# Kernel tuning notes

Hardware: AMD Instinct MI355X
Metric: run time of the kernel (lower is better)

Reference implementation:

```python
import jax, jax.numpy as jnp
import numpy as np

BLOCK = 128      # ModelArgs.block_size
FP8_MAX = 448.0  # e4m3 max, used by act_quant


def setup_inputs() -> dict:
    key = jax.random.key(0)
    k1, k2, k3 = jax.random.split(key, 3)
    M, K, O = 8192, 4096, 4096
    x = jax.random.normal(k1, (M, K), dtype=jnp.float32)
    # 'fp8' weight values (simulated in fp32) and blockwise fp32 scales
    weight = jax.random.normal(k2, (O, K), dtype=jnp.float32)
    w_scale = jax.random.uniform(k3, (O // BLOCK, K // BLOCK), dtype=jnp.float32,
                                 minval=0.5, maxval=1.5)
    return {"x": x, "weight": weight, "w_scale": w_scale}


def reference(x, weight, w_scale):
    M, K = x.shape
    O = weight.shape[0]
    Kb, Ob = K // BLOCK, O // BLOCK

    # --- act_quant: per-(row, k-block) scale = amax/448, quantized vals x/scale ---
    xb = x.reshape(M, Kb, BLOCK)
    sx = jnp.max(jnp.abs(xb), axis=-1, keepdims=True) / FP8_MAX  # [M, Kb, 1]
    xq = xb / sx                                                  # simulated fp8 activations

    # --- weight_dequant: blockwise scale expansion ---
    wdq = (weight.reshape(Ob, BLOCK, Kb, BLOCK) * w_scale[:, None, :, None]).reshape(O, K)

    # --- fp8_gemm: y = (xq * sx) @ wdq^T  (activation scales folded back per block) ---
    xd = (xq * sx).reshape(M, K)
    y = jnp.einsum('mk,ok->mo', xd, wdq)  # [M, O]
    return y
```

## Files before the change

### kernel.cpp

```cpp
#include <hip/hip_runtime.h>

#define M_DIM 8192
#define K_DIM 4096
#define O_DIM 4096
#define QB    128
#define BK    64
#define BMT   256
#define BNT   256

typedef __attribute__((ext_vector_type(8))) short  short8;
typedef __attribute__((ext_vector_type(4))) float  floatx4;

#define AS1 __attribute__((address_space(1)))
#define AS3 __attribute__((address_space(3)))

__device__ __forceinline__ short f2bf(float f) {
    unsigned u = __float_as_uint(f);
    unsigned r = u + 0x7fffu + ((u >> 16) & 1u);
    return (short)(r >> 16);
}

__global__ __launch_bounds__(512) void cvt_fused(const float* __restrict__ x,
                                                 const float* __restrict__ w,
                                                 const float* __restrict__ s,
                                                 short* __restrict__ xb,
                                                 short* __restrict__ wb) {
    const size_t NX = (size_t)M_DIM * K_DIM / 8;
    size_t t = (size_t)blockIdx.x * 512 + threadIdx.x;
    if (t < NX) {
        size_t i = t * 8;
        floatx4 f0 = *(const floatx4*)(x + i);
        floatx4 f1 = *(const floatx4*)(x + i + 4);
        short8 o;
        o[0] = f2bf(f0[0]); o[1] = f2bf(f0[1]); o[2] = f2bf(f0[2]); o[3] = f2bf(f0[3]);
        o[4] = f2bf(f1[0]); o[5] = f2bf(f1[1]); o[6] = f2bf(f1[2]); o[7] = f2bf(f1[3]);
        *(short8*)(xb + i) = o;
    } else {
        size_t i = (t - NX) * 8;
        int o = (int)(i >> 12);
        int k = (int)(i & (K_DIM - 1));
        float sc = s[(o >> 7) * (K_DIM / QB) + (k >> 7)];
        floatx4 f0 = *(const floatx4*)(w + i);
        floatx4 f1 = *(const floatx4*)(w + i + 4);
        short8 v;
        v[0] = f2bf(f0[0] * sc); v[1] = f2bf(f0[1] * sc);
        v[2] = f2bf(f0[2] * sc); v[3] = f2bf(f0[3] * sc);
        v[4] = f2bf(f1[0] * sc); v[5] = f2bf(f1[1] * sc);
        v[6] = f2bf(f1[2] * sc); v[7] = f2bf(f1[3] * sc);
        *(short8*)(wb + i) = v;
    }
}

#define WLG12 asm volatile("s_waitcnt lgkmcnt(12)" ::: "memory")
#define WLG8  asm volatile("s_waitcnt lgkmcnt(8)" ::: "memory")
#define WLG0  asm volatile("s_waitcnt lgkmcnt(0)" ::: "memory")
#define WVM2  asm volatile("s_waitcnt vmcnt(2)" ::: "memory")
#define WVM0  asm volatile("s_waitcnt vmcnt(0)" ::: "memory")
#define BARR  __builtin_amdgcn_s_barrier()
#define SCHEDB __builtin_amdgcn_sched_barrier(0)

#define LDA4(DST, BUF, ROFF)                                                    \
    _Pragma("unroll")                                                           \
    for (int mi = 0; mi < 4; ++mi) {                                            \
        DST[mi][0] = *(const short8*)&lsA[BUF][rA + (ROFF) + mi * 1024 + pc0];  \
        DST[mi][1] = *(const short8*)&lsA[BUF][rA + (ROFF) + mi * 1024 + pc1];  \
    }

#define LDB2(DST, BUF, ROFF)                                                    \
    _Pragma("unroll")                                                           \
    for (int ni = 0; ni < 2; ++ni) {                                            \
        DST[ni][0] = *(const short8*)&lsB[BUF][rB + (ROFF) + ni * 1024 + pc0];  \
        DST[ni][1] = *(const short8*)&lsB[BUF][rB + (ROFF) + ni * 1024 + pc1];  \
    }

#define RDA0(B) LDA4(a0, B, 0)
#define RDA1(B) LDA4(a1, B, 4096)
#define RDB0(B) LDB2(b0, B, 0)
#define RDB1(B) LDB2(b1, B, 2048)

#define MM16(AF, BF, MO, NO)                                                    \
    _Pragma("unroll")                                                           \
    for (int mi = 0; mi < 4; ++mi)                                              \
        _Pragma("unroll")                                                       \
        for (int ni = 0; ni < 2; ++ni)                                          \
            _Pragma("unroll")                                                   \
            for (int ks = 0; ks < 2; ++ks)                                      \
                acc[(MO) + mi][(NO) + ni] = __builtin_amdgcn_mfma_f32_16x16x32_bf16( \
                    AF[mi][ks], BF[ni][ks], acc[(MO) + mi][(NO) + ni], 0, 0, 0);

#define STAGE(LS, BUF, GP, KOFF, H)                                             \
    __builtin_amdgcn_global_load_lds(                                           \
        (const AS1 void*)((GP) + (size_t)((H) * 128) * K_DIM + (KOFF)),         \
        (AS3 void*)&LS[BUF][(H) * 128 * BK + dst], 16, 0, 0);                   \
    __builtin_amdgcn_global_load_lds(                                           \
        (const AS1 void*)((GP) + (size_t)((H) * 128 + 64) * K_DIM + (KOFF)),    \
        (AS3 void*)&LS[BUF][((H) * 128 + 64) * BK + dst], 16, 0, 0);

#define PH(STAGES, WAITM, MFMAS)                                                \
    STAGES                                                                      \
    BARR; WAITM; SCHEDB;                                                        \
    __builtin_amdgcn_s_setprio(1);                                              \
    MFMAS                                                                       \
    __builtin_amdgcn_s_setprio(0);                                              \
    BARR; SCHEDB;

#define PH3(STAGES, VMW, READS, MFMAS)                                          \
    STAGES                                                                      \
    VMW; BARR; SCHEDB;                                                          \
    READS                                                                       \
    WLG12; SCHEDB;                                                              \
    __builtin_amdgcn_s_setprio(1);                                              \
    MFMAS                                                                       \
    __builtin_amdgcn_s_setprio(0);                                              \
    BARR; SCHEDB;

#define TILE(c, n, k1, k2)                                                      \
    RDB1(c); RDA1(c);                                                           \
    PH(STAGE(lsA, n, gA, k1, 1), WLG12, MM16(a0, b0, 0, 0))                     \
    PH(STAGE(lsB, n, gB, k1, 0), WLG8,  MM16(a0, b1, 0, 2))                     \
    PH(STAGE(lsB, n, gB, k1, 1), WLG0,  MM16(a1, b0, 4, 0))                     \
    PH3(STAGE(lsA, c, gA, k2, 0), WVM2, RDA0(n); RDB0(n);, MM16(a1, b1, 4, 2))

__global__ __launch_bounds__(512, 2) void gemm_bt(const short* __restrict__ A,
                                                  const short* __restrict__ B,
                                                  float* __restrict__ C) {
    __shared__ __align__(16) short lsA[2][BMT * BK];
    __shared__ __align__(16) short lsB[2][BNT * BK];

    const int tid  = threadIdx.x;
    const int lane = tid & 63;
    const int wave = tid >> 6;
    const int wr   = wave >> 2;
    const int wc   = wave & 3;

    const int id  = blockIdx.x;
    const int xcd = id & 7;
    const int j   = id >> 3;
    const int bm  = j >> 1;
    const int bn  = (xcd << 1) | (j & 1);

    const int sr  = tid >> 3;
    const int csw = ((tid & 7) ^ (sr & 7)) << 3;
    const int dst = tid * 8;
    const short* gA = A + (size_t)(bm * BMT + sr) * K_DIM + csw;
    const short* gB = B + (size_t)(bn * BNT + sr) * K_DIM + csw;

    const int frow = lane & 15;
    const int fc   = lane >> 4;
    const int fsw  = frow & 7;
    const int pc0  = (fc ^ fsw) << 3;
    const int pc1  = ((4 + fc) ^ fsw) << 3;
    const int rA   = (wr * 128 + frow) * BK;
    const int rB   = (wc * 64 + frow) * BK;

    floatx4 acc[8][4];
#pragma unroll
    for (int mi = 0; mi < 8; ++mi)
#pragma unroll
        for (int ni = 0; ni < 4; ++ni)
            acc[mi][ni] = (floatx4){0.f, 0.f, 0.f, 0.f};

    short8 a0[4][2], a1[4][2], b0[2][2], b1[2][2];

    STAGE(lsA, 0, gA, 0, 0)
    STAGE(lsA, 0, gA, 0, 1)
    STAGE(lsB, 0, gB, 0, 0)
    STAGE(lsB, 0, gB, 0, 1)
    STAGE(lsA, 1, gA, 64, 0)
    WVM2; BARR; SCHEDB;
    RDA0(0); RDB0(0);

#pragma unroll 1
    for (int it = 0; it < 31; ++it) {
        TILE(0, 1, 64, 128)
        TILE(1, 0, 128, 192)
        gA += 128;
        gB += 128;
    }

    RDB1(0); RDA1(0);
    PH(STAGE(lsA, 1, gA, 64, 1), WLG12, MM16(a0, b0, 0, 0))
    PH(STAGE(lsB, 1, gB, 64, 0), WLG8,  MM16(a0, b1, 0, 2))
    PH(STAGE(lsB, 1, gB, 64, 1), WLG0,  MM16(a1, b0, 4, 0))
    PH3(, WVM0, RDA0(1); RDB0(1);, MM16(a1, b1, 4, 2))

    RDB1(1); RDA1(1);
    PH(, WLG12, MM16(a0, b0, 0, 0))
    PH(, WLG8,  MM16(a0, b1, 0, 2))
    PH(, WLG0,  MM16(a1, b0, 4, 0))
    SCHEDB;
    __builtin_amdgcn_s_setprio(1);
    MM16(a1, b1, 4, 2)
    __builtin_amdgcn_s_setprio(0);

    const int quad  = lane >> 4;
    const int crow0 = bm * BMT + wr * 128 + quad * 4;
    const int ccol0 = bn * BNT + wc * 64 + frow;
#pragma unroll
    for (int mi = 0; mi < 8; ++mi)
#pragma unroll
        for (int ni = 0; ni < 4; ++ni) {
            float* cp = C + (size_t)(crow0 + mi * 16) * O_DIM + (ccol0 + ni * 16);
#pragma unroll
            for (int r = 0; r < 4; ++r)
                cp[(size_t)r * O_DIM] = acc[mi][ni][r];
        }
}

extern "C" void kernel_launch(void* const* d_in, const int* in_sizes, int n_in,
                              void* d_out, int out_size, void* d_ws, size_t ws_size,
                              hipStream_t stream) {
    const float* x  = (const float*)d_in[0];
    const float* w  = (const float*)d_in[1];
    const float* ws = (const float*)d_in[2];
    float* out = (float*)d_out;

    short* xb = (short*)d_ws;
    short* wb = xb + (size_t)M_DIM * K_DIM;

    const size_t total_t = ((size_t)M_DIM * K_DIM + (size_t)O_DIM * K_DIM) / 8;
    cvt_fused<<<(unsigned)(total_t / 512), 512, 0, stream>>>(x, w, ws, xb, wb);

    gemm_bt<<<(M_DIM / BMT) * (O_DIM / BNT), 512, 0, stream>>>(xb, wb, out);
}
```

Baseline: 491.7 us.

## Reorder GEMM prefetch schedule and split conversion into grid-stride kernels

The GEMM main loop is restructured so that B tiles are prefetched one stage further ahead: the prologue stages B for the second buffer, and the order of global-to-LDS stages in each phase changes, with the vmcnt wait relaxed from 2 to 4. The intent is to keep more loads in flight and hide global latency behind the MFMAs. The single fused conversion kernel is split into separate grid-stride kernels for x and for w, each launched with 2048 blocks of 256 threads. The split adds one kernel launch and changes occupancy, and the reordered waits risk stalls or hazards if the counts are off.

```diff
diff --git a/kernel.cpp b/kernel.cpp
--- a/kernel.cpp
+++ b/kernel.cpp
@@ -20,14 +20,11 @@
     return (short)(r >> 16);
 }
 
-__global__ __launch_bounds__(512) void cvt_fused(const float* __restrict__ x,
-                                                 const float* __restrict__ w,
-                                                 const float* __restrict__ s,
-                                                 short* __restrict__ xb,
-                                                 short* __restrict__ wb) {
-    const size_t NX = (size_t)M_DIM * K_DIM / 8;
-    size_t t = (size_t)blockIdx.x * 512 + threadIdx.x;
-    if (t < NX) {
+__global__ __launch_bounds__(256) void cvt_x(const float* __restrict__ x,
+                                             short* __restrict__ xb) {
+    const size_t N8 = (size_t)M_DIM * K_DIM / 8;
+    const size_t stride = (size_t)gridDim.x * 256;
+    for (size_t t = (size_t)blockIdx.x * 256 + threadIdx.x; t < N8; t += stride) {
         size_t i = t * 8;
         floatx4 f0 = *(const floatx4*)(x + i);
         floatx4 f1 = *(const floatx4*)(x + i + 4);
@@ -35,8 +32,16 @@
         o[0] = f2bf(f0[0]); o[1] = f2bf(f0[1]); o[2] = f2bf(f0[2]); o[3] = f2bf(f0[3]);
         o[4] = f2bf(f1[0]); o[5] = f2bf(f1[1]); o[6] = f2bf(f1[2]); o[7] = f2bf(f1[3]);
         *(short8*)(xb + i) = o;
-    } else {
-        size_t i = (t - NX) * 8;
+    }
+}
+
+__global__ __launch_bounds__(256) void cvt_w(const float* __restrict__ w,
+                                             const float* __restrict__ s,
+                                             short* __restrict__ wb) {
+    const size_t N8 = (size_t)O_DIM * K_DIM / 8;
+    const size_t stride = (size_t)gridDim.x * 256;
+    for (size_t t = (size_t)blockIdx.x * 256 + threadIdx.x; t < N8; t += stride) {
+        size_t i = t * 8;
         int o = (int)(i >> 12);
         int k = (int)(i & (K_DIM - 1));
         float sc = s[(o >> 7) * (K_DIM / QB) + (k >> 7)];
@@ -54,10 +59,12 @@
 #define WLG12 asm volatile("s_waitcnt lgkmcnt(12)" ::: "memory")
 #define WLG8  asm volatile("s_waitcnt lgkmcnt(8)" ::: "memory")
 #define WLG0  asm volatile("s_waitcnt lgkmcnt(0)" ::: "memory")
-#define WVM2  asm volatile("s_waitcnt vmcnt(2)" ::: "memory")
+#define WVM4  asm volatile("s_waitcnt vmcnt(4)" ::: "memory")
 #define WVM0  asm volatile("s_waitcnt vmcnt(0)" ::: "memory")
 #define BARR  __builtin_amdgcn_s_barrier()
 #define SCHEDB __builtin_amdgcn_sched_barrier(0)
+#define SP1   __builtin_amdgcn_s_setprio(1)
+#define SP0   __builtin_amdgcn_s_setprio(0)
 
 #define LDA4(DST, BUF, ROFF)                                                    \
     _Pragma("unroll")                                                           \
@@ -96,30 +103,7 @@
         (const AS1 void*)((GP) + (size_t)((H) * 128 + 64) * K_DIM + (KOFF)),    \
         (AS3 void*)&LS[BUF][((H) * 128 + 64) * BK + dst], 16, 0, 0);
 
-#define PH(STAGES, WAITM, MFMAS)                                                \
-    STAGES                                                                      \
-    BARR; WAITM; SCHEDB;                                                        \
-    __builtin_amdgcn_s_setprio(1);                                              \
-    MFMAS                                                                       \
-    __builtin_amdgcn_s_setprio(0);                                              \
-    BARR; SCHEDB;
-
-#define PH3(STAGES, VMW, READS, MFMAS)                                          \
-    STAGES                                                                      \
-    VMW; BARR; SCHEDB;                                                          \
-    READS                                                                       \
-    WLG12; SCHEDB;                                                              \
-    __builtin_amdgcn_s_setprio(1);                                              \
-    MFMAS                                                                       \
-    __builtin_amdgcn_s_setprio(0);                                              \
-    BARR; SCHEDB;
-
-#define TILE(c, n, k1, k2)                                                      \
-    RDB1(c); RDA1(c);                                                           \
-    PH(STAGE(lsA, n, gA, k1, 1), WLG12, MM16(a0, b0, 0, 0))                     \
-    PH(STAGE(lsB, n, gB, k1, 0), WLG8,  MM16(a0, b1, 0, 2))                     \
-    PH(STAGE(lsB, n, gB, k1, 1), WLG0,  MM16(a1, b0, 4, 0))                     \
-    PH3(STAGE(lsA, c, gA, k2, 0), WVM2, RDA0(n); RDB0(n);, MM16(a1, b1, 4, 2))
+#define MF(WAIT, Q) BARR; WAIT; SCHEDB; SP1; Q SP0; BARR; SCHEDB;
 
 __global__ __launch_bounds__(512, 2) void gemm_bt(const short* __restrict__ A,
                                                   const short* __restrict__ B,
@@ -166,32 +150,56 @@
     STAGE(lsA, 0, gA, 0, 1)
     STAGE(lsB, 0, gB, 0, 0)
     STAGE(lsB, 0, gB, 0, 1)
-    STAGE(lsA, 1, gA, 64, 0)
-    WVM2; BARR; SCHEDB;
+    STAGE(lsB, 1, gB, 64, 0)
+    STAGE(lsB, 1, gB, 64, 1)
+    WVM4; BARR; SCHEDB;
     RDA0(0); RDB0(0);
 
 #pragma unroll 1
     for (int it = 0; it < 31; ++it) {
-        TILE(0, 1, 64, 128)
-        TILE(1, 0, 128, 192)
+        RDB1(0); RDA1(0);
+        STAGE(lsA, 1, gA, 64, 0)
+        MF(WLG12, MM16(a0, b0, 0, 0))
+        STAGE(lsA, 1, gA, 64, 1)
+        MF(WLG8,  MM16(a0, b1, 0, 2))
+        STAGE(lsB, 0, gB, 128, 0)
+        MF(WLG0,  MM16(a1, b0, 4, 0))
+        STAGE(lsB, 0, gB, 128, 1)
+        WVM4; BARR; SCHEDB;
+        RDA0(1); RDB0(1);
+        WLG12; SCHEDB; SP1; MM16(a1, b1, 4, 2) SP0; BARR; SCHEDB;
+
+        RDB1(1); RDA1(1);
+        STAGE(lsA, 0, gA, 128, 0)
+        MF(WLG12, MM16(a0, b0, 0, 0))
+        STAGE(lsA, 0, gA, 128, 1)
+        MF(WLG8,  MM16(a0, b1, 0, 2))
+        STAGE(lsB, 1, gB, 192, 0)
+        MF(WLG0,  MM16(a1, b0, 4, 0))
+        STAGE(lsB, 1, gB, 192, 1)
+        WVM4; BARR; SCHEDB;
+        RDA0(0); RDB0(0);
+        WLG12; SCHEDB; SP1; MM16(a1, b1, 4, 2) SP0; BARR; SCHEDB;
+
         gA += 128;
         gB += 128;
     }
 
     RDB1(0); RDA1(0);
-    PH(STAGE(lsA, 1, gA, 64, 1), WLG12, MM16(a0, b0, 0, 0))
-    PH(STAGE(lsB, 1, gB, 64, 0), WLG8,  MM16(a0, b1, 0, 2))
-    PH(STAGE(lsB, 1, gB, 64, 1), WLG0,  MM16(a1, b0, 4, 0))
-    PH3(, WVM0, RDA0(1); RDB0(1);, MM16(a1, b1, 4, 2))
+    STAGE(lsA, 1, gA, 64, 0)
+    MF(WLG12, MM16(a0, b0, 0, 0))
+    STAGE(lsA, 1, gA, 64, 1)
+    MF(WLG8,  MM16(a0, b1, 0, 2))
+    MF(WLG0,  MM16(a1, b0, 4, 0))
+    WVM0; BARR; SCHEDB;
+    RDA0(1); RDB0(1);
+    WLG12; SCHEDB; SP1; MM16(a1, b1, 4, 2) SP0; BARR; SCHEDB;
 
     RDB1(1); RDA1(1);
-    PH(, WLG12, MM16(a0, b0, 0, 0))
-    PH(, WLG8,  MM16(a0, b1, 0, 2))
-    PH(, WLG0,  MM16(a1, b0, 4, 0))
-    SCHEDB;
-    __builtin_amdgcn_s_setprio(1);
-    MM16(a1, b1, 4, 2)
-    __builtin_amdgcn_s_setprio(0);
+    MF(WLG12, MM16(a0, b0, 0, 0))
+    MF(WLG8,  MM16(a0, b1, 0, 2))
+    MF(WLG0,  MM16(a1, b0, 4, 0))
+    SCHEDB; SP1; MM16(a1, b1, 4, 2) SP0;
 
     const int quad  = lane >> 4;
     const int crow0 = bm * BMT + wr * 128 + quad * 4;
@@ -218,8 +226,8 @@
     short* xb = (short*)d_ws;
     short* wb = xb + (size_t)M_DIM * K_DIM;
 
-    const size_t total_t = ((size_t)M_DIM * K_DIM + (size_t)O_DIM * K_DIM) / 8;
-    cvt_fused<<<(unsigned)(total_t / 512), 512, 0, stream>>>(x, w, ws, xb, wb);
+    cvt_x<<<2048, 256, 0, stream>>>(x, xb);
+    cvt_w<<<2048, 256, 0, stream>>>(w, ws, wb);
 
     gemm_bt<<<(M_DIM / BMT) * (O_DIM / BNT), 512, 0, stream>>>(xb, wb, out);
 }
```

Result: slower. 508.7 us (+3.5%).
